# Kernel tuning notes

Measured on AMD Instinct MI355X. Metric: run time of the kernel, lower is better.

The kernel has to match this reference:

```python
import jax, jax.numpy as jnp
import numpy as np

DIM = 1024
NUM_HEADS = 16
HEAD_DIM = DIM // NUM_HEADS


def apply_rotary_embed(x, thetas):
    # x: (..., seq, d), thetas: (seq, d) broadcast over leading dims
    x1, x2 = jnp.split(x, 2, axis=-1)
    x_rot = jnp.concatenate([-x2, x1], axis=-1)
    return x * jnp.cos(thetas) + x_rot * jnp.sin(thetas)


def setup_inputs() -> dict:
    key = jax.random.key(0)
    ks = jax.random.split(key, 8)
    B, Nx, Nc = 4, 1024, 2048
    x = jax.random.normal(ks[0], (B, Nx, DIM), dtype=jnp.float32)
    c = jax.random.normal(ks[1], (B, Nc, DIM), dtype=jnp.float32)
    x_pos_embed = jax.random.normal(ks[2], (Nx, HEAD_DIM), dtype=jnp.float32)
    c_pos_embed = jax.random.normal(ks[3], (Nc, HEAD_DIM), dtype=jnp.float32)
    s = 1.0 / np.sqrt(DIM)
    Wq = jax.random.normal(ks[4], (DIM, DIM), dtype=jnp.float32) * s
    Wkv = jax.random.normal(ks[5], (DIM, 2 * DIM), dtype=jnp.float32) * s
    Wproj = jax.random.normal(ks[6], (DIM, DIM), dtype=jnp.float32) * s
    bproj = jnp.zeros((DIM,), dtype=jnp.float32)
    return {"x": x, "c": c, "x_pos_embed": x_pos_embed, "c_pos_embed": c_pos_embed,
            "Wq": Wq, "Wkv": Wkv, "Wproj": Wproj, "bproj": bproj}


def reference(x, c, x_pos_embed, c_pos_embed, Wq, Wkv, Wproj, bproj):
    B, Nx, D = x.shape
    Nc = c.shape[1]
    H, hd = NUM_HEADS, HEAD_DIM
    # Q projection -> (B, H, Nx, hd)
    q = (x @ Wq).reshape(B, Nx, H, hd).transpose(0, 2, 1, 3)
    q = apply_rotary_embed(q, x_pos_embed)
    # KV projection -> k, v each (B, H, Nc, hd)
    kv = (c @ Wkv).reshape(B, Nc, 2, H, hd).transpose(2, 0, 3, 1, 4)
    k, v = kv[0], kv[1]
    k = apply_rotary_embed(k, c_pos_embed)
    # scaled dot-product attention (dropout p=0 -> identity)
    scale = 1.0 / np.sqrt(hd).astype(np.float32)
    attn = jnp.einsum('bhqd,bhkd->bhqk', q, k) * scale
    attn = jax.nn.softmax(attn, axis=-1)
    out = jnp.einsum('bhqk,bhkd->bhqd', attn, v)
    out = out.transpose(0, 2, 1, 3).reshape(B, Nx, D)
    return out @ Wproj + bproj
```

## Files before the change

### kernel.cpp

```cpp
#include <hip/hip_runtime.h>
#include <math.h>

#define DIMC  1024
#define NHEAD 16
#define HD    64
#define NB    4
#define NX    1024
#define NC    2048
#define KD    1024

typedef _Float16 half_t;
typedef __attribute__((ext_vector_type(8))) _Float16 h8;
typedef __attribute__((ext_vector_type(4))) _Float16 h4;
typedef __attribute__((ext_vector_type(2))) __fp16 fp16x2;
typedef __attribute__((ext_vector_type(4))) float f32x4;

#define QSCALE 0.1803368801111244f
#define NEGM  -8.656170245333781f

__device__ __forceinline__ void gload_lds16(const half_t* g, half_t* l) {
    __builtin_amdgcn_global_load_lds(
        (__attribute__((address_space(1))) void*)(g),
        (__attribute__((address_space(3))) void*)(l), 16, 0, 0);
}

__device__ __forceinline__ void wtile(const float* __restrict__ W,
                                      half_t* __restrict__ Wt, int N,
                                      int bx, int by, int t)
{
    __shared__ half_t T[64][72];
    const int k0 = by * 64, n0 = bx * 64;
    const int kr = t >> 2, c0 = (t & 3) << 4;
    const float* src = W + (size_t)(k0 + kr) * N + n0 + c0;
#pragma unroll
    for (int j = 0; j < 16; j += 4) {
        float4 v = *(const float4*)(src + j);
        T[c0 + j + 0][kr] = (half_t)v.x;
        T[c0 + j + 1][kr] = (half_t)v.y;
        T[c0 + j + 2][kr] = (half_t)v.z;
        T[c0 + j + 3][kr] = (half_t)v.w;
    }
    __syncthreads();
    const int nr = t >> 2, kc = (t & 3) << 4;
    half_t* dst = Wt + (size_t)(n0 + nr) * KD + k0 + kc;
    *(int4*)dst       = *(const int4*)&T[nr][kc];
    *(int4*)(dst + 8) = *(const int4*)&T[nr][kc + 8];
}

__global__ __launch_bounds__(256) void prep(
    const float* __restrict__ x, half_t* __restrict__ xh,
    const float* __restrict__ c, half_t* __restrict__ ch,
    const float* __restrict__ xpe, const float* __restrict__ cpe,
    float* __restrict__ xct, float* __restrict__ xst,
    float* __restrict__ cct, float* __restrict__ cst,
    const float* __restrict__ Wq,  half_t* __restrict__ Wqt,
    const float* __restrict__ Wkv, half_t* __restrict__ Wkt,
    const float* __restrict__ Wp,  half_t* __restrict__ Wpt)
{
    const int bid = blockIdx.x, t = threadIdx.x;
    if (bid < 1024) {
        if (bid < 256)      wtile(Wq,  Wqt, DIMC,     bid & 15,         bid >> 4,         t);
        else if (bid < 768) wtile(Wkv, Wkt, 2 * DIMC, (bid - 256) & 31, (bid - 256) >> 5, t);
        else                wtile(Wp,  Wpt, DIMC,     (bid - 768) & 15, (bid - 768) >> 4, t);
    } else if (bid < 7168) {
        const int nx = NB * NX * DIMC;
        const int i = ((bid - 1024) * 256 + t) * 8;
        const float* s;
        half_t* d;
        if (i < nx) { s = x + i; d = xh + i; }
        else        { s = c + (i - nx); d = ch + (i - nx); }
        float4 a = *(const float4*)(s);
        float4 b = *(const float4*)(s + 4);
        h8 o;
        o[0] = (half_t)a.x; o[1] = (half_t)a.y; o[2] = (half_t)a.z; o[3] = (half_t)a.w;
        o[4] = (half_t)b.x; o[5] = (half_t)b.y; o[6] = (half_t)b.z; o[7] = (half_t)b.w;
        *(h8*)d = o;
    } else {
        const int i = (bid - 7168) * 256 + t;
        if (i < NX * HD) {
            const float th = xpe[i];
            xct[i] = cosf(th); xst[i] = sinf(th);
        } else {
            const int j = i - NX * HD;
            const float th = cpe[j];
            cct[j] = cosf(th); cst[j] = sinf(th);
        }
    }
}

template <int MODE, int BN>
__global__ __launch_bounds__(256) void hgemm(
    const half_t* __restrict__ Ag, const half_t* __restrict__ Bt,
    const float* __restrict__ ct, const float* __restrict__ st,
    const float* __restrict__ bias,
    void* __restrict__ out0, void* __restrict__ out1)
{
    constexpr int MI = (BN == 128) ? 4 : 2;
    constexpr int BLOADS = BN / 32;
    __shared__ half_t As[2][8192];
    __shared__ half_t Bs[2][BN * 64];

    const int tid = threadIdx.x;
    const int w = tid >> 6, lane = tid & 63;
    const int lr = lane & 15, lg = lane >> 4;
    const int wrOff = (BN == 128) ? (w >> 1) * 64 : w * 32;
    const int wcOff = (BN == 128) ? (w & 1) * 64 : 0;

    int lin = (int)blockIdx.x;
    lin = (lin & 7) * ((int)gridDim.x >> 3) + (lin >> 3);
    const int m0 = (lin >> 4) * 128, n0 = (lin & 15) * BN;

    f32x4 acc[MI][4];
#pragma unroll
    for (int i = 0; i < MI; ++i)
#pragma unroll
        for (int j = 0; j < 4; ++j) acc[i][j] = f32x4{0.f, 0.f, 0.f, 0.f};

    size_t gA[4], gB[BLOADS];
    int loff[4];
#pragma unroll
    for (int c = 0; c < 4; ++c) {
        const int L = c * 4096 + w * 1024 + lane * 16;
        const int row = L >> 7;
        const int ss = ((L >> 4) & 7) ^ (row & 7);
        gA[c] = (size_t)(m0 + row) * KD + ss * 8;
        if (c < BLOADS) gB[c] = (size_t)(n0 + row) * KD + ss * 8;
        loff[c] = c * 2048 + w * 512;
    }

#define HSTAGE(buf, kk) do {                                               \
        _Pragma("unroll")                                                  \
        for (int c = 0; c < 4; ++c) {                                      \
            gload_lds16(Ag + gA[c] + (kk) * 64, &As[buf][loff[c]]);        \
            if (c < BLOADS) gload_lds16(Bt + gB[c] + (kk) * 64, &Bs[buf][loff[c]]); \
        }                                                                  \
    } while (0)

    HSTAGE(0, 0);
    asm volatile("s_waitcnt vmcnt(0)" ::: "memory");
    __builtin_amdgcn_s_barrier();
    __builtin_amdgcn_sched_barrier(0);

    for (int k = 0; k < KD / 64; ++k) {
        const int cb = k & 1;
        if (k + 1 < KD / 64) {
            HSTAGE(cb ^ 1, k + 1);
            if constexpr (BLOADS == 4)
                asm volatile("s_waitcnt vmcnt(8)" ::: "memory");
            else
                asm volatile("s_waitcnt vmcnt(6)" ::: "memory");
        } else {
            asm volatile("s_waitcnt vmcnt(0)" ::: "memory");
        }
        __builtin_amdgcn_s_barrier();
        __builtin_amdgcn_sched_barrier(0);

        __builtin_amdgcn_s_setprio(1);
#pragma unroll
        for (int kc = 0; kc < 2; ++kc) {
            h8 af[MI], bf[4];
#pragma unroll
            for (int mi = 0; mi < MI; ++mi) {
                const int r = wrOff + mi * 16 + lr;
                af[mi] = *(const h8*)&As[cb][r * 64 + (((kc * 4 + lg) ^ (r & 7)) << 3)];
            }
#pragma unroll
            for (int ni = 0; ni < 4; ++ni) {
                const int r = wcOff + ni * 16 + lr;
                bf[ni] = *(const h8*)&Bs[cb][r * 64 + (((kc * 4 + lg) ^ (r & 7)) << 3)];
            }
#pragma unroll
            for (int mi = 0; mi < MI; ++mi)
#pragma unroll
                for (int ni = 0; ni < 4; ++ni)
                    acc[mi][ni] = __builtin_amdgcn_mfma_f32_16x16x32_f16(
                        af[mi], bf[ni], acc[mi][ni], 0, 0, 0);
        }
        __builtin_amdgcn_s_setprio(0);

        __builtin_amdgcn_s_barrier();
        __builtin_amdgcn_sched_barrier(0);
    }
#undef HSTAGE

    if (MODE == 2) {
        float* o = (float*)out0;
#pragma unroll
        for (int ni = 0; ni < 4; ++ni) {
            const int col = n0 + ni * 16 + lr;
            const float bv = bias[col];
#pragma unroll
            for (int mi = 0; mi < MI; ++mi)
#pragma unroll
                for (int r = 0; r < 4; ++r) {
                    const int row = m0 + wrOff + mi * 16 + lg * 4 + r;
                    o[(size_t)row * DIMC + col] = acc[mi][ni][r] + bv;
                }
        }
        return;
    }

    if (MODE == 0) {
        half_t* Qw = (half_t*)out0;
        const int h = n0 >> 6;
#pragma unroll
        for (int mi = 0; mi < MI; ++mi)
#pragma unroll
            for (int r = 0; r < 4; ++r) {
                const int row = m0 + wrOff + mi * 16 + lg * 4 + r;
                const int bb = row >> 10, nn = row & (NX - 1);
                const float* cr = ct + nn * HD;
                const float* sr = st + nn * HD;
                half_t* op = Qw + (((size_t)(bb * NHEAD + h)) * NX + nn) * HD;
#pragma unroll
                for (int ni = 0; ni < 4; ++ni) {
                    const int d = ni * 16 + lr;
                    const float val = acc[mi][ni][r];
                    const float pv  = acc[mi][ni ^ 2][r];
                    op[d] = (half_t)((val * cr[d] + (ni < 2 ? -pv : pv) * sr[d]) * QSCALE);
                }
            }
    } else {
        const bool isK = (n0 < DIMC);
        const int h = ((n0 & (DIMC - 1)) >> 6) + (w & 1);
        half_t* Kw = (half_t*)out0;
        half_t* Vw = (half_t*)out1;
#pragma unroll
        for (int mi = 0; mi < MI; ++mi)
#pragma unroll
            for (int r = 0; r < 4; ++r) {
                const int row = m0 + wrOff + mi * 16 + lg * 4 + r;
                const int bb = row >> 11, nn = row & (NC - 1);
                const int tt = nn >> 6, rr = nn & 63;
                const size_t tbase = ((size_t)(bb * NHEAD + h) * 32 + tt) * 4096;
                const float* cr = ct + nn * HD;
                const float* sr = st + nn * HD;
#pragma unroll
                for (int ni = 0; ni < 4; ++ni) {
                    const int d = ni * 16 + lr;
                    const float val = acc[mi][ni][r];
                    if (isK) {
                        const float pv = acc[mi][ni ^ 2][r];
                        Kw[tbase + rr * 64 + ((((d >> 3) ^ (rr & 7)) << 3) | (d & 7))] =
                            (half_t)(val * cr[d] + (ni < 2 ? -pv : pv) * sr[d]);
                    } else {
                        Vw[tbase + d * 64 + ((((rr >> 3) ^ (d & 7)) << 3) | (rr & 7))] =
                            (half_t)val;
                    }
                }
            }
    }
}

__global__ __launch_bounds__(256) void attn_mfma(
    const half_t* __restrict__ Q, const half_t* __restrict__ Kg,
    const half_t* __restrict__ Vg, half_t* __restrict__ O)
{
    __shared__ half_t Ks[2][4096];
    __shared__ half_t Vs[2][4096];
    __shared__ half_t Ps[4096];

    const int tid = threadIdx.x;
    const int w = tid >> 6, lane = tid & 63;
    const int lr = lane & 15, lg = lane >> 4;
    const int e7 = lr & 7;

    const int sid = (blockIdx.x & 7) * 128 + (blockIdx.x >> 3);
    const int bh = sid >> 4;
    const int q0 = (sid & 15) * 64;
    const int b = bh >> 4, h = bh & 15;

    const half_t* qbase = Q + ((size_t)bh * NX + q0 + w * 16 + lr) * HD + lg * 8;
    const h8 qf0 = *(const h8*)(qbase);
    const h8 qf1 = *(const h8*)(qbase + 32);

    f32x4 acc[4];
#pragma unroll
    for (int i = 0; i < 4; ++i) acc[i] = f32x4{0.f, 0.f, 0.f, 0.f};
    f32x4 accl = {0.f, 0.f, 0.f, 0.f};

    h8 vone;
#pragma unroll
    for (int i = 0; i < 8; ++i) vone[i] = (half_t)(lr == 0 ? 1.0f : 0.0f);

    const half_t* Kt = Kg + (size_t)bh * 32 * 4096;
    const half_t* Vt = Vg + (size_t)bh * 32 * 4096;
    const int so = w * 512 + lane * 8;

#define STAGE(bi, t) do {                                           \
        const half_t* kg_ = Kt + (size_t)(t) * 4096;                \
        const half_t* vg_ = Vt + (size_t)(t) * 4096;                \
        gload_lds16(kg_ + so,        &Ks[bi][w * 512]);             \
        gload_lds16(kg_ + 2048 + so, &Ks[bi][2048 + w * 512]);      \
        gload_lds16(vg_ + so,        &Vs[bi][w * 512]);             \
        gload_lds16(vg_ + 2048 + so, &Vs[bi][2048 + w * 512]);      \
    } while (0)

    STAGE(0, 0);
    asm volatile("s_waitcnt vmcnt(0)" ::: "memory");
    __builtin_amdgcn_s_barrier();
    __builtin_amdgcn_sched_barrier(0);

    const int rowq = w * 16 + lr;

    for (int t = 0; t < NC / 64; ++t) {
        const int cur = t & 1;
        if (t + 1 < NC / 64) {
            STAGE(cur ^ 1, t + 1);
            asm volatile("s_waitcnt vmcnt(8)" ::: "memory");
        } else {
            asm volatile("s_waitcnt vmcnt(0)" ::: "memory");
        }
        __builtin_amdgcn_s_barrier();
        __builtin_amdgcn_sched_barrier(0);

        f32x4 sc[4];
        __builtin_amdgcn_s_setprio(1);
#pragma unroll
        for (int cb = 0; cb < 4; ++cb) {
            const int r = cb * 16 + lr;
            const h8 kf0 = *(const h8*)&Ks[cur][r * 64 + ((lg ^ e7) << 3)];
            const h8 kf1 = *(const h8*)&Ks[cur][r * 64 + (((4 + lg) ^ e7) << 3)];
            f32x4 a = {NEGM, NEGM, NEGM, NEGM};
            a = __builtin_amdgcn_mfma_f32_16x16x32_f16(kf0, qf0, a, 0, 0, 0);
            a = __builtin_amdgcn_mfma_f32_16x16x32_f16(kf1, qf1, a, 0, 0, 0);
            sc[cb] = a;
        }
        __builtin_amdgcn_s_setprio(0);

#pragma unroll
        for (int cb = 0; cb < 4; ++cb) {
            fp16x2 a01 = __builtin_amdgcn_cvt_pkrtz(exp2f(sc[cb][0]), exp2f(sc[cb][1]));
            fp16x2 a23 = __builtin_amdgcn_cvt_pkrtz(exp2f(sc[cb][2]), exp2f(sc[cb][3]));
            union { h4 h; uint2 u; } pw;
            pw.u.x = *(unsigned int*)&a01;
            pw.u.y = *(unsigned int*)&a23;
            const int s = cb * 2 + (lg >> 1);
            *(h4*)&Ps[rowq * 64 + ((s ^ e7) << 3) + (lg & 1) * 4] = pw.h;
        }

        const h8 pf0 = *(const h8*)&Ps[rowq * 64 + ((lg ^ e7) << 3)];
        const h8 pf1 = *(const h8*)&Ps[rowq * 64 + (((4 + lg) ^ e7) << 3)];
        __builtin_amdgcn_s_setprio(1);
#pragma unroll
        for (int db = 0; db < 4; ++db) {
            const int rd = db * 16 + lr;
            const h8 vf0 = *(const h8*)&Vs[cur][rd * 64 + ((lg ^ e7) << 3)];
            const h8 vf1 = *(const h8*)&Vs[cur][rd * 64 + (((4 + lg) ^ e7) << 3)];
            acc[db] = __builtin_amdgcn_mfma_f32_16x16x32_f16(pf0, vf0, acc[db], 0, 0, 0);
            acc[db] = __builtin_amdgcn_mfma_f32_16x16x32_f16(pf1, vf1, acc[db], 0, 0, 0);
        }
        accl = __builtin_amdgcn_mfma_f32_16x16x32_f16(pf0, vone, accl, 0, 0, 0);
        accl = __builtin_amdgcn_mfma_f32_16x16x32_f16(pf1, vone, accl, 0, 0, 0);
        __builtin_amdgcn_s_setprio(0);

        __builtin_amdgcn_s_barrier();
        __builtin_amdgcn_sched_barrier(0);
    }
#undef STAGE

    float invs[4];
#pragma unroll
    for (int r = 0; r < 4; ++r)
        invs[r] = 1.f / __shfl(accl[r], lg << 4);

    half_t* Ob = O + ((size_t)b * NX + q0 + w * 16) * DIMC + h * HD;
#pragma unroll
    for (int db = 0; db < 4; ++db)
#pragma unroll
        for (int r = 0; r < 4; ++r)
            Ob[(size_t)(lg * 4 + r) * DIMC + db * 16 + lr] =
                (half_t)(acc[db][r] * invs[r]);
}

extern "C" void kernel_launch(void* const* d_in, const int* in_sizes, int n_in,
                              void* d_out, int out_size, void* d_ws, size_t ws_size,
                              hipStream_t stream)
{
    const float* x     = (const float*)d_in[0];
    const float* c     = (const float*)d_in[1];
    const float* xpe   = (const float*)d_in[2];
    const float* cpe   = (const float*)d_in[3];
    const float* Wq    = (const float*)d_in[4];
    const float* Wkv   = (const float*)d_in[5];
    const float* Wproj = (const float*)d_in[6];
    const float* bproj = (const float*)d_in[7];

    char* wsb = (char*)d_ws;
    half_t* xh  = (half_t*)(wsb);
    half_t* ch  = (half_t*)(wsb + ((size_t)8  << 20));
    half_t* Wqt = (half_t*)(wsb + ((size_t)24 << 20));
    half_t* Wkt = (half_t*)(wsb + ((size_t)26 << 20));
    half_t* Wpt = (half_t*)(wsb + ((size_t)30 << 20));
    half_t* Kw  = (half_t*)(wsb + ((size_t)32 << 20));
    half_t* Vw  = (half_t*)(wsb + ((size_t)48 << 20));
    half_t* Ow  = (half_t*)(wsb + ((size_t)64 << 20));
    float*  xct = (float*)(wsb + ((size_t)72 << 20));
    float*  xst = (float*)(wsb + ((size_t)72 << 20) + (256u << 10));
    float*  cct = (float*)(wsb + ((size_t)72 << 20) + (512u << 10));
    float*  cst = (float*)(wsb + ((size_t)72 << 20) + (1024u << 10));
    half_t* Qw  = (half_t*)d_out;

    prep<<<7936, 256, 0, stream>>>(x, xh, c, ch, xpe, cpe,
                                   xct, xst, cct, cst,
                                   Wq, Wqt, Wkv, Wkt, Wproj, Wpt);

    hgemm<0, 64><<<512, 256, 0, stream>>>(xh, Wqt, xct, xst, nullptr,
                                          Qw, nullptr);
    hgemm<1, 128><<<1024, 256, 0, stream>>>(ch, Wkt, cct, cst, nullptr,
                                            Kw, Vw);
    attn_mfma<<<1024, 256, 0, stream>>>(Qw, Kw, Vw, Ow);
    hgemm<2, 64><<<512, 256, 0, stream>>>(Ow, Wpt, nullptr, nullptr, bproj,
                                          (float*)d_out, nullptr);
}
```

Before: 188.8 us.

## Add dedicated 256x256-tile KV GEMM with pre-swizzled tiled operand images

Replaces the generic KV projection GEMM with a specialised 512-thread kernel using 256x256 output tiles, 8 waves, and a hand-scheduled double-buffered pipeline built on direct global-to-LDS loads with explicit vmcnt gating and priority hints. The prep kernel now writes c and Wkv in a pre-tiled, XOR-swizzled layout so each K-chunk tile is contiguous and can be streamed straight into LDS. The aim is more reuse per loaded byte and better overlap of loads with MFMA work. In exchange it uses 128KB of LDS and many accumulator registers per block, which limits occupancy and makes the hand schedule fragile.

```diff
diff --git a/kernel.cpp b/kernel.cpp
--- a/kernel.cpp
+++ b/kernel.cpp
@@ -25,7 +25,7 @@
 }
 
 __device__ __forceinline__ void wtile(const float* __restrict__ W,
-                                      half_t* __restrict__ Wt, int N,
+                                      half_t* __restrict__ Wt, int N, int IMG,
                                       int bx, int by, int t)
 {
     __shared__ half_t T[64][72];
@@ -42,9 +42,18 @@
     }
     __syncthreads();
     const int nr = t >> 2, kc = (t & 3) << 4;
-    half_t* dst = Wt + (size_t)(n0 + nr) * KD + k0 + kc;
-    *(int4*)dst       = *(const int4*)&T[nr][kc];
-    *(int4*)(dst + 8) = *(const int4*)&T[nr][kc + 8];
+    if (!IMG) {
+        half_t* dst = Wt + (size_t)(n0 + nr) * KD + k0 + kc;
+        *(int4*)dst       = *(const int4*)&T[nr][kc];
+        *(int4*)(dst + 8) = *(const int4*)&T[nr][kc + 8];
+    } else {
+        const int n = n0 + nr;
+        const int ntile = n >> 8, rr = n & 255;
+        const int s0 = kc >> 3;
+        half_t* base = Wt + ((size_t)(ntile * 16 + by) * 256 + rr) * 64;
+        *(int4*)(base + ((s0 ^ (rr & 7)) << 3))       = *(const int4*)&T[nr][kc];
+        *(int4*)(base + (((s0 + 1) ^ (rr & 7)) << 3)) = *(const int4*)&T[nr][kc + 8];
+    }
 }
 
 __global__ __launch_bounds__(256) void prep(
@@ -59,22 +68,32 @@
 {
     const int bid = blockIdx.x, t = threadIdx.x;
     if (bid < 1024) {
-        if (bid < 256)      wtile(Wq,  Wqt, DIMC,     bid & 15,         bid >> 4,         t);
-        else if (bid < 768) wtile(Wkv, Wkt, 2 * DIMC, (bid - 256) & 31, (bid - 256) >> 5, t);
-        else                wtile(Wp,  Wpt, DIMC,     (bid - 768) & 15, (bid - 768) >> 4, t);
+        if (bid < 256)      wtile(Wq,  Wqt, DIMC, 0,     bid & 15,         bid >> 4,         t);
+        else if (bid < 768) wtile(Wkv, Wkt, 2 * DIMC, 1, (bid - 256) & 31, (bid - 256) >> 5, t);
+        else                wtile(Wp,  Wpt, DIMC, 0,     (bid - 768) & 15, (bid - 768) >> 4, t);
     } else if (bid < 7168) {
         const int nx = NB * NX * DIMC;
         const int i = ((bid - 1024) * 256 + t) * 8;
         const float* s;
-        half_t* d;
-        if (i < nx) { s = x + i; d = xh + i; }
-        else        { s = c + (i - nx); d = ch + (i - nx); }
-        float4 a = *(const float4*)(s);
-        float4 b = *(const float4*)(s + 4);
         h8 o;
-        o[0] = (half_t)a.x; o[1] = (half_t)a.y; o[2] = (half_t)a.z; o[3] = (half_t)a.w;
-        o[4] = (half_t)b.x; o[5] = (half_t)b.y; o[6] = (half_t)b.z; o[7] = (half_t)b.w;
-        *(h8*)d = o;
+        if (i < nx) {
+            s = x + i;
+            float4 a = *(const float4*)(s);
+            float4 b = *(const float4*)(s + 4);
+            o[0] = (half_t)a.x; o[1] = (half_t)a.y; o[2] = (half_t)a.z; o[3] = (half_t)a.w;
+            o[4] = (half_t)b.x; o[5] = (half_t)b.y; o[6] = (half_t)b.z; o[7] = (half_t)b.w;
+            *(h8*)(xh + i) = o;
+        } else {
+            const int j = i - nx;
+            s = c + j;
+            float4 a = *(const float4*)(s);
+            float4 b = *(const float4*)(s + 4);
+            o[0] = (half_t)a.x; o[1] = (half_t)a.y; o[2] = (half_t)a.z; o[3] = (half_t)a.w;
+            o[4] = (half_t)b.x; o[5] = (half_t)b.y; o[6] = (half_t)b.z; o[7] = (half_t)b.w;
+            const int R = j >> 10, k = j & 1023;
+            const int mt = R >> 8, r = R & 255, kt = k >> 6, sl = (k & 63) >> 3;
+            *(h8*)(ch + ((size_t)(mt * 16 + kt) * 256 + r) * 64 + ((sl ^ (r & 7)) << 3)) = o;
+        }
     } else {
         const int i = (bid - 7168) * 256 + t;
         if (i < NX * HD) {
@@ -220,36 +239,146 @@
                     op[d] = (half_t)((val * cr[d] + (ni < 2 ? -pv : pv) * sr[d]) * QSCALE);
                 }
             }
-    } else {
-        const bool isK = (n0 < DIMC);
-        const int h = ((n0 & (DIMC - 1)) >> 6) + (w & 1);
-        half_t* Kw = (half_t*)out0;
-        half_t* Vw = (half_t*)out1;
-#pragma unroll
-        for (int mi = 0; mi < MI; ++mi)
-#pragma unroll
-            for (int r = 0; r < 4; ++r) {
-                const int row = m0 + wrOff + mi * 16 + lg * 4 + r;
-                const int bb = row >> 11, nn = row & (NC - 1);
-                const int tt = nn >> 6, rr = nn & 63;
-                const size_t tbase = ((size_t)(bb * NHEAD + h) * 32 + tt) * 4096;
-                const float* cr = ct + nn * HD;
-                const float* sr = st + nn * HD;
-#pragma unroll
-                for (int ni = 0; ni < 4; ++ni) {
-                    const int d = ni * 16 + lr;
-                    const float val = acc[mi][ni][r];
-                    if (isK) {
-                        const float pv = acc[mi][ni ^ 2][r];
-                        Kw[tbase + rr * 64 + ((((d >> 3) ^ (rr & 7)) << 3) | (d & 7))] =
-                            (half_t)(val * cr[d] + (ni < 2 ? -pv : pv) * sr[d]);
-                    } else {
-                        Vw[tbase + d * 64 + ((((rr >> 3) ^ (d & 7)) << 3) | (rr & 7))] =
-                            (half_t)val;
-                    }
+    }
+}
+
+__global__ __launch_bounds__(512, 2) void hgemm_kv(
+    const half_t* __restrict__ Aimg, const half_t* __restrict__ Bimg,
+    const float* __restrict__ ct, const float* __restrict__ st,
+    half_t* __restrict__ Kw, half_t* __restrict__ Vw)
+{
+    __shared__ half_t lds[65536];
+
+    const int tid = threadIdx.x;
+    const int w = tid >> 6, lane = tid & 63;
+    const int lr = lane & 15, lg = lane >> 4;
+    const int wr = w >> 2, wc = w & 3;
+    const int wrOff = wr * 128, wcOff = wc * 64;
+
+    int lin = (int)blockIdx.x;
+    lin = (lin & 7) * 32 + (lin >> 3);
+    const int mt = lin >> 3, nt = lin & 7;
+    const int m0 = mt * 256, n0 = nt * 256;
+
+    const half_t* Ablk = Aimg + (size_t)mt * 262144;
+    const half_t* Bblk = Bimg + (size_t)nt * 262144;
+    const int so2 = w * 512 + lane * 8;
+
+    f32x4 acc[8][4];
+#pragma unroll
+    for (int i = 0; i < 8; ++i)
+#pragma unroll
+        for (int j = 0; j < 4; ++j) acc[i][j] = f32x4{0.f, 0.f, 0.f, 0.f};
+    h8 af[2][2];
+    h8 bf[4][2];
+
+#define ISSUEH(SRC, DSTOFF) do {                                     \
+        gload_lds16((SRC) + so2,        &lds[(DSTOFF) + w * 512]);   \
+        gload_lds16((SRC) + 4096 + so2, &lds[(DSTOFF) + 4096 + w * 512]); \
+    } while (0)
+
+#define PHASE(MI0, AOFF, BOFF, READBF, STG, GATE) do {               \
+        _Pragma("unroll")                                            \
+        for (int kc = 0; kc < 2; ++kc)                               \
+        _Pragma("unroll")                                            \
+        for (int d = 0; d < 2; ++d) {                                \
+            const int r_ = wrOff + ((MI0) + d) * 16 + lr;            \
+            af[d][kc] = *(const h8*)&lds[(AOFF) + r_ * 64 + (((kc * 4 + lg) ^ (r_ & 7)) << 3)]; \
+        }                                                            \
+        if (READBF) {                                                \
+            _Pragma("unroll")                                        \
+            for (int ni = 0; ni < 4; ++ni)                           \
+            _Pragma("unroll")                                        \
+            for (int kc = 0; kc < 2; ++kc) {                         \
+                const int rb = wcOff + ni * 16 + lr;                 \
+                bf[ni][kc] = *(const h8*)&lds[(BOFF) + rb * 64 + (((kc * 4 + lg) ^ (rb & 7)) << 3)]; \
+            }                                                        \
+        }                                                            \
+        STG;                                                         \
+        __builtin_amdgcn_sched_barrier(0);                           \
+        __builtin_amdgcn_s_barrier();                                \
+        __builtin_amdgcn_s_setprio(1);                               \
+        _Pragma("unroll")                                            \
+        for (int d = 0; d < 2; ++d)                                  \
+        _Pragma("unroll")                                            \
+        for (int ni = 0; ni < 4; ++ni)                               \
+        _Pragma("unroll")                                            \
+        for (int kc = 0; kc < 2; ++kc)                               \
+            acc[(MI0) + d][ni] = __builtin_amdgcn_mfma_f32_16x16x32_f16( \
+                af[d][kc], bf[ni][kc], acc[(MI0) + d][ni], 0, 0, 0); \
+        __builtin_amdgcn_s_setprio(0);                               \
+        GATE;                                                        \
+        __builtin_amdgcn_s_barrier();                                \
+    } while (0)
+
+#define GATE4 asm volatile("s_waitcnt vmcnt(4)" ::: "memory")
+#define GATE0 asm volatile("s_waitcnt vmcnt(0)" ::: "memory")
+#define NOG   ((void)0)
+
+    ISSUEH(Ablk, 0);          ISSUEH(Ablk + 8192, 8192);
+    ISSUEH(Bblk, 32768);      ISSUEH(Bblk + 8192, 32768 + 8192);
+    __builtin_amdgcn_sched_barrier(0);
+    ISSUEH(Bblk + 16384, 49152); ISSUEH(Bblk + 16384 + 8192, 49152 + 8192);
+    asm volatile("s_waitcnt vmcnt(4)" ::: "memory");
+    __builtin_amdgcn_s_barrier();
+
+    for (int i = 0; i < 7; ++i) {
+        const half_t* An1 = Ablk + (size_t)(2 * i + 1) * 16384;
+        const half_t* An2 = Ablk + (size_t)(2 * i + 2) * 16384;
+        const half_t* Bn2 = Bblk + (size_t)(2 * i + 2) * 16384;
+        const half_t* Bn3 = Bblk + (size_t)(2 * i + 3) * 16384;
+        PHASE(0, 0,     32768, true,  ISSUEH(An1, 16384),               NOG);
+        PHASE(2, 0,     32768, false, ISSUEH(An1 + 8192, 16384 + 8192), NOG);
+        PHASE(4, 0,     32768, false, ISSUEH(Bn2, 32768),               NOG);
+        PHASE(6, 0,     32768, false, ISSUEH(Bn2 + 8192, 32768 + 8192), GATE4);
+        PHASE(0, 16384, 49152, true,  ISSUEH(An2, 0),                   NOG);
+        PHASE(2, 16384, 49152, false, ISSUEH(An2 + 8192, 8192),         NOG);
+        PHASE(4, 16384, 49152, false, ISSUEH(Bn3, 49152),               NOG);
+        PHASE(6, 16384, 49152, false, ISSUEH(Bn3 + 8192, 49152 + 8192), GATE4);
+    }
+    {
+        const half_t* A15 = Ablk + (size_t)15 * 16384;
+        PHASE(0, 0,     32768, true,  ISSUEH(A15, 16384),               NOG);
+        PHASE(2, 0,     32768, false, ISSUEH(A15 + 8192, 16384 + 8192), NOG);
+        PHASE(4, 0,     32768, false, NOG,                              NOG);
+        PHASE(6, 0,     32768, false, NOG,                              GATE0);
+        PHASE(0, 16384, 49152, true,  NOG,                              NOG);
+        PHASE(2, 16384, 49152, false, NOG,                              NOG);
+        PHASE(4, 16384, 49152, false, NOG,                              NOG);
+        PHASE(6, 16384, 49152, false, NOG,                              NOG);
+    }
+#undef PHASE
+#undef ISSUEH
+#undef GATE4
+#undef GATE0
+#undef NOG
+
+    const bool isK = (n0 < DIMC);
+    const int h = ((n0 & (DIMC - 1)) >> 6) + wc;
+#pragma unroll
+    for (int mi = 0; mi < 8; ++mi)
+#pragma unroll
+        for (int r = 0; r < 4; ++r) {
+            const int row = m0 + wrOff + mi * 16 + lg * 4 + r;
+            const int bb = row >> 11, nn = row & (NC - 1);
+            const int tt = nn >> 6, rr = nn & 63;
+            const size_t tbase = ((size_t)(bb * NHEAD + h) * 32 + tt) * 4096;
+            const float* cr = ct + nn * HD;
+            const float* sr = st + nn * HD;
+#pragma unroll
+            for (int ni = 0; ni < 4; ++ni) {
+                const int d = ni * 16 + lr;
+                const float val = acc[mi][ni][r];
+                if (isK) {
+                    const float pv = acc[mi][ni ^ 2][r];
+                    Kw[tbase + rr * 64 + ((((d >> 3) ^ (rr & 7)) << 3) | (d & 7))] =
+                        (half_t)(val * cr[d] + (ni < 2 ? -pv : pv) * sr[d]);
+                } else {
+                    Vw[tbase + d * 64 + ((((rr >> 3) ^ (d & 7)) << 3) | (rr & 7))] =
+                        (half_t)val;
                 }
             }
-    }
+        }
 }
 
 __global__ __launch_bounds__(256) void attn_mfma(
@@ -407,8 +536,7 @@
 
     hgemm<0, 64><<<512, 256, 0, stream>>>(xh, Wqt, xct, xst, nullptr,
                                           Qw, nullptr);
-    hgemm<1, 128><<<1024, 256, 0, stream>>>(ch, Wkt, cct, cst, nullptr,
-                                            Kw, Vw);
+    hgemm_kv<<<256, 512, 0, stream>>>(ch, Wkt, cct, cst, Kw, Vw);
     attn_mfma<<<1024, 256, 0, stream>>>(Qw, Kw, Vw, Ow);
     hgemm<2, 64><<<512, 256, 0, stream>>>(Ow, Wpt, nullptr, nullptr, bproj,
                                           (float*)d_out, nullptr);
```

After: 184.8 us. -2.1%, faster.
